# Kernel optimization log

Hardware: AMD Instinct MI355X
Metric: run time of the kernel (lower is better)

## Reference

```python
import jax, jax.numpy as jnp
import numpy as np

IN_FEATURES = 4096
OUT_FEATURES = 11008
GROUP_SIZE = 128
N_HIGH = 1024   # int(0.25*4096)//8*8
N_LOW = 3072    # (4096-1024)//8*8
M_TOKENS = 64


def unpack_6bit(packed, original_k):
    # packed: [K*3//4, N] uint8 values stored as int32
    _, N = packed.shape
    p = packed.reshape(original_k // 4, 3, N)
    b0, b1, b2 = p[:, 0], p[:, 1], p[:, 2]
    v0 = b0 & 63
    v1 = ((b0 >> 6) & 3) | ((b1 & 15) << 2)
    v2 = ((b1 >> 4) & 15) | ((b2 & 3) << 4)
    v3 = (b2 >> 2) & 63
    return jnp.stack([v0, v1, v2, v3], axis=1).reshape(original_k, N)


def unpack_5bit(packed, original_k):
    # packed: [K*5//8, N]
    _, N = packed.shape
    p = packed.reshape(original_k // 8, 5, N)
    b = [p[:, i] for i in range(5)]
    v0 = b[0] & 31
    v1 = ((b[0] >> 5) & 7) | ((b[1] & 3) << 3)
    v2 = (b[1] >> 2) & 31
    v3 = ((b[1] >> 7) & 1) | ((b[2] & 15) << 1)
    v4 = ((b[2] >> 4) & 15) | ((b[3] & 1) << 4)
    v5 = (b[3] >> 1) & 31
    v6 = ((b[3] >> 6) & 3) | ((b[4] & 7) << 2)
    v7 = (b[4] >> 3) & 31
    return jnp.stack([v0, v1, v2, v3, v4, v5, v6, v7], axis=1).reshape(original_k, N)


def dequant_region(W_q, scales, half_range):
    # W_q: [K, N] ints in [0, 2*half_range]; scales: [num_groups, N]
    K, N = W_q.shape
    G = scales.shape[0]
    Wg = (W_q.astype(jnp.float32) - float(half_range)).reshape(G, GROUP_SIZE, N)
    return (Wg * scales[:, None, :]).reshape(K, N)


def setup_inputs() -> dict:
    key = jax.random.key(0)
    ks = jax.random.split(key, 7)
    x = jax.random.normal(ks[0], (M_TOKENS, IN_FEATURES), dtype=jnp.float32)
    W_high_packed = jax.random.randint(ks[1], (N_HIGH * 3 // 4, OUT_FEATURES), 0, 256, dtype=jnp.int32)
    W_low_packed = jax.random.randint(ks[2], (N_LOW * 5 // 8, OUT_FEATURES), 0, 256, dtype=jnp.int32)
    scales_high = jax.random.uniform(ks[3], (N_HIGH // GROUP_SIZE, OUT_FEATURES), dtype=jnp.float32) * 0.02 + 1e-4
    scales_low = jax.random.uniform(ks[4], (N_LOW // GROUP_SIZE, OUT_FEATURES), dtype=jnp.float32) * 0.02 + 1e-4
    col_indices = jax.random.permutation(ks[5], IN_FEATURES).astype(jnp.int32)
    bias = jax.random.normal(ks[6], (OUT_FEATURES,), dtype=jnp.float32) * 0.02
    return {"x": x, "W_high_packed": W_high_packed, "W_low_packed": W_low_packed,
            "scales_high": scales_high, "scales_low": scales_low,
            "col_indices": col_indices, "bias": bias}


def reference(x, W_high_packed, W_low_packed, scales_high, scales_low, col_indices, bias):
    # Unpack mixed 6-bit / 5-bit weights and group-dequantize.
    Wq_high = unpack_6bit(W_high_packed, N_HIGH)          # [1024, N], 0..63
    Wq_low = unpack_5bit(W_low_packed, N_LOW)             # [3072, N], 0..31
    W_high = dequant_region(Wq_high, scales_high, 31)     # 6-bit half_range = 31
    W_low = dequant_region(Wq_low, scales_low, 15)        # 5-bit half_range = 15
    # Column-sensitivity reorder of activations, then split high/low regions.
    x_perm = x[:, col_indices]                            # [M, K]
    x_high = x_perm[:, :N_HIGH]
    x_low = x_perm[:, N_HIGH:N_HIGH + N_LOW]
    out = x_high @ W_high + x_low @ W_low + bias          # [M, N]
    return out
```

## Files before the change

kernel.cpp:

```cpp
#include <hip/hip_runtime.h>


#define NFEAT 11008
#define KTOT  4096

typedef _Float16 half8 __attribute__((ext_vector_type(8)));
typedef float    f32x4 __attribute__((ext_vector_type(4)));

__global__ __launch_bounds__(256) void prep_xfrag(const float* __restrict__ x,
                                                  const int* __restrict__ col,
                                                  _Float16* __restrict__ xfrag) {
    int idx = blockIdx.x * 256 + threadIdx.x;
    int j  = idx & 7;
    int l  = (idx >> 3) & 63;
    int mt = (idx >> 9) & 3;
    int s  = idx >> 11;
    int k  = s * 32 + ((l >> 4) << 3) + j;
    int m  = mt * 16 + (l & 15);
    xfrag[idx] = (_Float16)x[m * KTOT + col[k]];
}

__global__ __launch_bounds__(512) void gemm_kernel(const int* __restrict__ Wh,
                                                   const int* __restrict__ Wl,
                                                   const float* __restrict__ sh,
                                                   const float* __restrict__ sl,
                                                   const _Float16* __restrict__ xfrag,
                                                   float* __restrict__ dst,
                                                   int atomic_mode) {
    const int n0   = blockIdx.x * 64;
    const int kc   = blockIdx.y;
    const int tid  = threadIdx.x;
    const int lane = tid & 63;
    const int wave = tid >> 6;

    __shared__ _Float16 Wfrag[2][8 * 64 * 8 + 4 * 8];

    f32x4 acc[4];
#pragma unroll
    for (int i = 0; i < 4; ++i) acc[i] = (f32x4){0.f, 0.f, 0.f, 0.f};

    const int col  = lane;
    const int nt   = col >> 4;
    const int n_in = col & 15;
    const int kg   = wave;
    const int q_w  = kg >> 2, quad = kg & 3;
    const int woff = (((nt * 2 + q_w) * 64 + quad * 16 + n_in) + nt) * 8;

    const int mt = wave & 3;
    const int qm = wave >> 2;

    auto mfma_step = [&](int t) {
        const int sg = kc * 32 + t * 2 + qm;
        half8 a = *(const half8*)(xfrag + (((sg * 4 + mt) * 64 + lane) << 3));
        const _Float16* wf = Wfrag[t & 1];
#pragma unroll
        for (int j = 0; j < 4; ++j) {
            half8 b = *(const half8*)&wf[(((j * 2 + qm) * 64 + lane) + j) * 8];
            acc[j] = __builtin_amdgcn_mfma_f32_16x16x32_f16(a, b, acc[j], 0, 0, 0);
        }
    };

    if (kc == 0) {
        const int*   base  = Wh + n0 + col;
        const float* sbase = sh + n0 + col;
        int c0, c1, c2, c3, c4, c5; float cs;
        {
            const int* bp = base + 3 * (kg * 2) * NFEAT;
            c0 = bp[0];         c1 = bp[NFEAT];     c2 = bp[2 * NFEAT];
            c3 = bp[3 * NFEAT]; c4 = bp[4 * NFEAT]; c5 = bp[5 * NFEAT];
            cs = sbase[0];
        }
#pragma unroll 2
        for (int t = 0; t < 16; ++t) {
            int n_0 = 0, n_1 = 0, n_2 = 0, n_3 = 0, n_4 = 0, n_5 = 0; float ns = 0.f;
            if (t + 1 < 16) {
                const int G = (t + 1) * 16 + kg * 2;
                const int* bp = base + 3 * G * NFEAT;
                n_0 = bp[0];         n_1 = bp[NFEAT];     n_2 = bp[2 * NFEAT];
                n_3 = bp[3 * NFEAT]; n_4 = bp[4 * NFEAT]; n_5 = bp[5 * NFEAT];
                ns = sbase[((t + 1) >> 1) * NFEAT];
            }
            int v[8];
            v[0] = c0 & 63;
            v[1] = ((c0 >> 6) & 3) | ((c1 & 15) << 2);
            v[2] = ((c1 >> 4) & 15) | ((c2 & 3) << 4);
            v[3] = (c2 >> 2) & 63;
            v[4] = c3 & 63;
            v[5] = ((c3 >> 6) & 3) | ((c4 & 15) << 2);
            v[6] = ((c4 >> 4) & 15) | ((c5 & 3) << 4);
            v[7] = (c5 >> 2) & 63;
            half8 w;
#pragma unroll
            for (int j = 0; j < 8; ++j) w[j] = (_Float16)(((float)v[j] - 31.0f) * cs);
            *(half8*)&Wfrag[t & 1][woff] = w;
            __syncthreads();
            mfma_step(t);
            c0 = n_0; c1 = n_1; c2 = n_2; c3 = n_3; c4 = n_4; c5 = n_5; cs = ns;
        }
    } else {
        const int*   base  = Wl + n0 + col;
        const float* sbase = sl + n0 + col;
        const int Gbase = (kc - 1) * 128;
        const int sbase_row = (kc - 1) * 8;
        int c0, c1, c2, c3, c4; float cs;
        {
            const int* bp = base + 5 * (Gbase + kg) * NFEAT;
            c0 = bp[0]; c1 = bp[NFEAT]; c2 = bp[2 * NFEAT];
            c3 = bp[3 * NFEAT]; c4 = bp[4 * NFEAT];
            cs = sbase[sbase_row * NFEAT];
        }
#pragma unroll 2
        for (int t = 0; t < 16; ++t) {
            int n_0 = 0, n_1 = 0, n_2 = 0, n_3 = 0, n_4 = 0; float ns = 0.f;
            if (t + 1 < 16) {
                const int* bp = base + 5 * (Gbase + (t + 1) * 8 + kg) * NFEAT;
                n_0 = bp[0]; n_1 = bp[NFEAT]; n_2 = bp[2 * NFEAT];
                n_3 = bp[3 * NFEAT]; n_4 = bp[4 * NFEAT];
                ns = sbase[(sbase_row + ((t + 1) >> 1)) * NFEAT];
            }
            int v[8];
            v[0] = c0 & 31;
            v[1] = ((c0 >> 5) & 7) | ((c1 & 3) << 3);
            v[2] = (c1 >> 2) & 31;
            v[3] = ((c1 >> 7) & 1) | ((c2 & 15) << 1);
            v[4] = ((c2 >> 4) & 15) | ((c3 & 1) << 4);
            v[5] = (c3 >> 1) & 31;
            v[6] = ((c3 >> 6) & 3) | ((c4 & 7) << 2);
            v[7] = (c4 >> 3) & 31;
            half8 w;
#pragma unroll
            for (int j = 0; j < 8; ++j) w[j] = (_Float16)(((float)v[j] - 15.0f) * cs);
            *(half8*)&Wfrag[t & 1][woff] = w;
            __syncthreads();
            mfma_step(t);
            c0 = n_0; c1 = n_1; c2 = n_2; c3 = n_3; c4 = n_4; cs = ns;
        }
    }

    __syncthreads();
    float* red = (float*)&Wfrag[0][0];
    if (wave >= 4) {
#pragma unroll
        for (int j = 0; j < 4; ++j)
#pragma unroll
            for (int r = 0; r < 4; ++r)
                red[(j * 4 + r) * 256 + (wave - 4) * 64 + lane] = acc[j][r];
    }
    __syncthreads();
    if (wave < 4) {
#pragma unroll
        for (int j = 0; j < 4; ++j)
#pragma unroll
            for (int r = 0; r < 4; ++r)
                acc[j][r] += red[(j * 4 + r) * 256 + wave * 64 + lane];

        const int rb = wave * 16 + ((lane >> 4) << 2);
        const int cb = lane & 15;
        if (atomic_mode) {
#pragma unroll
            for (int j = 0; j < 4; ++j)
#pragma unroll
                for (int r = 0; r < 4; ++r)
                    atomicAdd(&dst[(rb + r) * NFEAT + n0 + j * 16 + cb], acc[j][r]);
        } else {
            float* base = dst + (size_t)kc * 64 * NFEAT;
#pragma unroll
            for (int j = 0; j < 4; ++j)
#pragma unroll
                for (int r = 0; r < 4; ++r)
                    base[(rb + r) * NFEAT + n0 + j * 16 + cb] = acc[j][r];
        }
    }
}

__global__ __launch_bounds__(256) void reduce_out(const float* __restrict__ part,
                                                  const float* __restrict__ bias,
                                                  float* __restrict__ out) {
    const int idx = blockIdx.x * 256 + threadIdx.x;
    const int f   = idx * 4;
    const int n   = f % NFEAT;
    f32x4 a = *(const f32x4*)(part + f);
    f32x4 b = *(const f32x4*)(part + 704512 + f);
    f32x4 c = *(const f32x4*)(part + 2 * 704512 + f);
    f32x4 d = *(const f32x4*)(part + 3 * 704512 + f);
    f32x4 bi = *(const f32x4*)(bias + n);
    *(f32x4*)(out + f) = a + b + c + d + bi;
}

__global__ __launch_bounds__(256) void init_bias(const float* __restrict__ bias,
                                                 float* __restrict__ out) {
    const int idx = blockIdx.x * 256 + threadIdx.x;
    out[idx] = bias[idx % NFEAT];
}

extern "C" void kernel_launch(void* const* d_in, const int* in_sizes, int n_in,
                              void* d_out, int out_size, void* d_ws, size_t ws_size,
                              hipStream_t stream) {
    const float* x    = (const float*)d_in[0];
    const int*   Wh   = (const int*)d_in[1];
    const int*   Wl   = (const int*)d_in[2];
    const float* sh   = (const float*)d_in[3];
    const float* sl   = (const float*)d_in[4];
    const int*   col  = (const int*)d_in[5];
    const float* bias = (const float*)d_in[6];
    float* out = (float*)d_out;

    _Float16* xfrag = (_Float16*)d_ws;
    const size_t xfrag_bytes = 64 * KTOT * sizeof(_Float16);
    const size_t part_bytes  = 4ull * 64 * NFEAT * sizeof(float);

    prep_xfrag<<<1024, 256, 0, stream>>>(x, col, xfrag);

    dim3 grid(172, 4);
    if (ws_size >= xfrag_bytes + part_bytes) {
        float* part = (float*)((char*)d_ws + xfrag_bytes);
        gemm_kernel<<<grid, 512, 0, stream>>>(Wh, Wl, sh, sl, xfrag, part, 0);
        reduce_out<<<688, 256, 0, stream>>>(part, bias, out);
    } else {
        init_bias<<<2752, 256, 0, stream>>>(bias, out);
        gemm_kernel<<<grid, 512, 0, stream>>>(Wh, Wl, sh, sl, xfrag, out, 1);
    }
}
```

Before: 175.0 us.

## Deepen weight prefetch to two stages and keep global loads in flight across barriers

Restructures the dequant-GEMM main loop into an explicit even/odd two-stage pipeline. Packed weights, scales and x fragments are prefetched two steps ahead instead of one. __syncthreads is replaced by a barrier that waits only on LDS counters, so outstanding global loads stay in flight across the barrier. The aim is to hide global-memory latency for the weight stream, at the cost of more registers and reliance on the LDS double buffer being safe without waiting on vmcnt.

Result: slower. 180.2 us (+3.0%).

```diff
diff --git a/kernel.cpp b/kernel.cpp
--- a/kernel.cpp
+++ b/kernel.cpp
@@ -6,6 +6,13 @@
 
 typedef _Float16 half8 __attribute__((ext_vector_type(8)));
 typedef float    f32x4 __attribute__((ext_vector_type(4)));
+
+#define BARRIER_KEEP_INFLIGHT()                                   \
+    do {                                                          \
+        asm volatile("s_waitcnt lgkmcnt(0)" ::: "memory");        \
+        __builtin_amdgcn_s_barrier();                             \
+        asm volatile("" ::: "memory");                            \
+    } while (0)
 
 __global__ __launch_bounds__(256) void prep_xfrag(const float* __restrict__ x,
                                                   const int* __restrict__ col,
@@ -49,10 +56,10 @@
     const int mt = wave & 3;
     const int qm = wave >> 2;
 
-    auto mfma_step = [&](int t) {
-        const int sg = kc * 32 + t * 2 + qm;
-        half8 a = *(const half8*)(xfrag + (((sg * 4 + mt) * 64 + lane) << 3));
-        const _Float16* wf = Wfrag[t & 1];
+    auto aoff = [&](int t) {
+        return (((kc * 32 + t * 2 + qm) * 4 + mt) * 64 + lane) << 3;
+    };
+    auto mfma4 = [&](const _Float16* wf, half8 a) {
 #pragma unroll
         for (int j = 0; j < 4; ++j) {
             half8 b = *(const half8*)&wf[(((j * 2 + qm) * 64 + lane) + j) * 8];
@@ -61,79 +68,138 @@
     };
 
     if (kc == 0) {
+        auto deq6 = [](int b0, int b1, int b2, int b3, int b4, int b5, float s) -> half8 {
+            int v0 = b0 & 63;
+            int v1 = ((b0 >> 6) & 3) | ((b1 & 15) << 2);
+            int v2 = ((b1 >> 4) & 15) | ((b2 & 3) << 4);
+            int v3 = (b2 >> 2) & 63;
+            int v4 = b3 & 63;
+            int v5 = ((b3 >> 6) & 3) | ((b4 & 15) << 2);
+            int v6 = ((b4 >> 4) & 15) | ((b5 & 3) << 4);
+            int v7 = (b5 >> 2) & 63;
+            half8 w;
+            w[0] = (_Float16)(((float)v0 - 31.0f) * s);
+            w[1] = (_Float16)(((float)v1 - 31.0f) * s);
+            w[2] = (_Float16)(((float)v2 - 31.0f) * s);
+            w[3] = (_Float16)(((float)v3 - 31.0f) * s);
+            w[4] = (_Float16)(((float)v4 - 31.0f) * s);
+            w[5] = (_Float16)(((float)v5 - 31.0f) * s);
+            w[6] = (_Float16)(((float)v6 - 31.0f) * s);
+            w[7] = (_Float16)(((float)v7 - 31.0f) * s);
+            return w;
+        };
         const int*   base  = Wh + n0 + col;
         const float* sbase = sh + n0 + col;
-        int c0, c1, c2, c3, c4, c5; float cs;
+        int A0, A1, A2, A3, A4, A5; float As;
+        int B0, B1, B2, B3, B4, B5; float Bs;
+        half8 xaE, xaO;
         {
             const int* bp = base + 3 * (kg * 2) * NFEAT;
-            c0 = bp[0];         c1 = bp[NFEAT];     c2 = bp[2 * NFEAT];
-            c3 = bp[3 * NFEAT]; c4 = bp[4 * NFEAT]; c5 = bp[5 * NFEAT];
-            cs = sbase[0];
-        }
-#pragma unroll 2
-        for (int t = 0; t < 16; ++t) {
-            int n_0 = 0, n_1 = 0, n_2 = 0, n_3 = 0, n_4 = 0, n_5 = 0; float ns = 0.f;
-            if (t + 1 < 16) {
-                const int G = (t + 1) * 16 + kg * 2;
-                const int* bp = base + 3 * G * NFEAT;
-                n_0 = bp[0];         n_1 = bp[NFEAT];     n_2 = bp[2 * NFEAT];
-                n_3 = bp[3 * NFEAT]; n_4 = bp[4 * NFEAT]; n_5 = bp[5 * NFEAT];
-                ns = sbase[((t + 1) >> 1) * NFEAT];
-            }
-            int v[8];
-            v[0] = c0 & 63;
-            v[1] = ((c0 >> 6) & 3) | ((c1 & 15) << 2);
-            v[2] = ((c1 >> 4) & 15) | ((c2 & 3) << 4);
-            v[3] = (c2 >> 2) & 63;
-            v[4] = c3 & 63;
-            v[5] = ((c3 >> 6) & 3) | ((c4 & 15) << 2);
-            v[6] = ((c4 >> 4) & 15) | ((c5 & 3) << 4);
-            v[7] = (c5 >> 2) & 63;
+            A0 = bp[0];         A1 = bp[NFEAT];     A2 = bp[2 * NFEAT];
+            A3 = bp[3 * NFEAT]; A4 = bp[4 * NFEAT]; A5 = bp[5 * NFEAT];
+            As = sbase[0];
+            bp = base + 3 * (16 + kg * 2) * NFEAT;
+            B0 = bp[0];         B1 = bp[NFEAT];     B2 = bp[2 * NFEAT];
+            B3 = bp[3 * NFEAT]; B4 = bp[4 * NFEAT]; B5 = bp[5 * NFEAT];
+            Bs = sbase[0];
+            xaE = *(const half8*)(xfrag + aoff(0));
+            xaO = *(const half8*)(xfrag + aoff(1));
+        }
+        for (int i = 0; i < 8; ++i) {
+            {
+                half8 w = deq6(A0, A1, A2, A3, A4, A5, As);
+                half8 acur = xaE;
+                *(half8*)&Wfrag[0][woff] = w;
+                const int tp = (i < 7) ? 2 * i + 2 : 14;
+                const int* bp = base + 3 * (tp * 16 + kg * 2) * NFEAT;
+                A0 = bp[0];         A1 = bp[NFEAT];     A2 = bp[2 * NFEAT];
+                A3 = bp[3 * NFEAT]; A4 = bp[4 * NFEAT]; A5 = bp[5 * NFEAT];
+                As = sbase[(tp >> 1) * NFEAT];
+                xaE = *(const half8*)(xfrag + aoff(tp));
+                BARRIER_KEEP_INFLIGHT();
+                mfma4(Wfrag[0], acur);
+            }
+            {
+                half8 w = deq6(B0, B1, B2, B3, B4, B5, Bs);
+                half8 acur = xaO;
+                *(half8*)&Wfrag[1][woff] = w;
+                const int tp = (i < 7) ? 2 * i + 3 : 15;
+                const int* bp = base + 3 * (tp * 16 + kg * 2) * NFEAT;
+                B0 = bp[0];         B1 = bp[NFEAT];     B2 = bp[2 * NFEAT];
+                B3 = bp[3 * NFEAT]; B4 = bp[4 * NFEAT]; B5 = bp[5 * NFEAT];
+                Bs = sbase[(tp >> 1) * NFEAT];
+                xaO = *(const half8*)(xfrag + aoff(tp));
+                BARRIER_KEEP_INFLIGHT();
+                mfma4(Wfrag[1], acur);
+            }
+        }
+    } else {
+        auto deq5 = [](int b0, int b1, int b2, int b3, int b4, float s) -> half8 {
+            int v0 = b0 & 31;
+            int v1 = ((b0 >> 5) & 7) | ((b1 & 3) << 3);
+            int v2 = (b1 >> 2) & 31;
+            int v3 = ((b1 >> 7) & 1) | ((b2 & 15) << 1);
+            int v4 = ((b2 >> 4) & 15) | ((b3 & 1) << 4);
+            int v5 = (b3 >> 1) & 31;
+            int v6 = ((b3 >> 6) & 3) | ((b4 & 7) << 2);
+            int v7 = (b4 >> 3) & 31;
             half8 w;
-#pragma unroll
-            for (int j = 0; j < 8; ++j) w[j] = (_Float16)(((float)v[j] - 31.0f) * cs);
-            *(half8*)&Wfrag[t & 1][woff] = w;
-            __syncthreads();
-            mfma_step(t);
-            c0 = n_0; c1 = n_1; c2 = n_2; c3 = n_3; c4 = n_4; c5 = n_5; cs = ns;
-        }
-    } else {
+            w[0] = (_Float16)(((float)v0 - 15.0f) * s);
+            w[1] = (_Float16)(((float)v1 - 15.0f) * s);
+            w[2] = (_Float16)(((float)v2 - 15.0f) * s);
+            w[3] = (_Float16)(((float)v3 - 15.0f) * s);
+            w[4] = (_Float16)(((float)v4 - 15.0f) * s);
+            w[5] = (_Float16)(((float)v5 - 15.0f) * s);
+            w[6] = (_Float16)(((float)v6 - 15.0f) * s);
+            w[7] = (_Float16)(((float)v7 - 15.0f) * s);
+            return w;
+        };
         const int*   base  = Wl + n0 + col;
         const float* sbase = sl + n0 + col;
-        const int Gbase = (kc - 1) * 128;
+        const int Gbase     = (kc - 1) * 128;
         const int sbase_row = (kc - 1) * 8;
-        int c0, c1, c2, c3, c4; float cs;
+        int A0, A1, A2, A3, A4; float As;
+        int B0, B1, B2, B3, B4; float Bs;
+        half8 xaE, xaO;
         {
             const int* bp = base + 5 * (Gbase + kg) * NFEAT;
-            c0 = bp[0]; c1 = bp[NFEAT]; c2 = bp[2 * NFEAT];
-            c3 = bp[3 * NFEAT]; c4 = bp[4 * NFEAT];
-            cs = sbase[sbase_row * NFEAT];
-        }
-#pragma unroll 2
-        for (int t = 0; t < 16; ++t) {
-            int n_0 = 0, n_1 = 0, n_2 = 0, n_3 = 0, n_4 = 0; float ns = 0.f;
-            if (t + 1 < 16) {
-                const int* bp = base + 5 * (Gbase + (t + 1) * 8 + kg) * NFEAT;
-                n_0 = bp[0]; n_1 = bp[NFEAT]; n_2 = bp[2 * NFEAT];
-                n_3 = bp[3 * NFEAT]; n_4 = bp[4 * NFEAT];
-                ns = sbase[(sbase_row + ((t + 1) >> 1)) * NFEAT];
-            }
-            int v[8];
-            v[0] = c0 & 31;
-            v[1] = ((c0 >> 5) & 7) | ((c1 & 3) << 3);
-            v[2] = (c1 >> 2) & 31;
-            v[3] = ((c1 >> 7) & 1) | ((c2 & 15) << 1);
-            v[4] = ((c2 >> 4) & 15) | ((c3 & 1) << 4);
-            v[5] = (c3 >> 1) & 31;
-            v[6] = ((c3 >> 6) & 3) | ((c4 & 7) << 2);
-            v[7] = (c4 >> 3) & 31;
-            half8 w;
-#pragma unroll
-            for (int j = 0; j < 8; ++j) w[j] = (_Float16)(((float)v[j] - 15.0f) * cs);
-            *(half8*)&Wfrag[t & 1][woff] = w;
-            __syncthreads();
-            mfma_step(t);
-            c0 = n_0; c1 = n_1; c2 = n_2; c3 = n_3; c4 = n_4; cs = ns;
+            A0 = bp[0]; A1 = bp[NFEAT]; A2 = bp[2 * NFEAT];
+            A3 = bp[3 * NFEAT]; A4 = bp[4 * NFEAT];
+            As = sbase[sbase_row * NFEAT];
+            bp = base + 5 * (Gbase + 8 + kg) * NFEAT;
+            B0 = bp[0]; B1 = bp[NFEAT]; B2 = bp[2 * NFEAT];
+            B3 = bp[3 * NFEAT]; B4 = bp[4 * NFEAT];
+            Bs = sbase[sbase_row * NFEAT];
+            xaE = *(const half8*)(xfrag + aoff(0));
+            xaO = *(const half8*)(xfrag + aoff(1));
+        }
+        for (int i = 0; i < 8; ++i) {
+            {
+                half8 w = deq5(A0, A1, A2, A3, A4, As);
+                half8 acur = xaE;
+                *(half8*)&Wfrag[0][woff] = w;
+                const int tp = (i < 7) ? 2 * i + 2 : 14;
+                const int* bp = base + 5 * (Gbase + tp * 8 + kg) * NFEAT;
+                A0 = bp[0]; A1 = bp[NFEAT]; A2 = bp[2 * NFEAT];
+                A3 = bp[3 * NFEAT]; A4 = bp[4 * NFEAT];
+                As = sbase[(sbase_row + (tp >> 1)) * NFEAT];
+                xaE = *(const half8*)(xfrag + aoff(tp));
+                BARRIER_KEEP_INFLIGHT();
+                mfma4(Wfrag[0], acur);
+            }
+            {
+                half8 w = deq5(B0, B1, B2, B3, B4, Bs);
+                half8 acur = xaO;
+                *(half8*)&Wfrag[1][woff] = w;
+                const int tp = (i < 7) ? 2 * i + 3 : 15;
+                const int* bp = base + 5 * (Gbase + tp * 8 + kg) * NFEAT;
+                B0 = bp[0]; B1 = bp[NFEAT]; B2 = bp[2 * NFEAT];
+                B3 = bp[3 * NFEAT]; B4 = bp[4 * NFEAT];
+                Bs = sbase[(sbase_row + (tp >> 1)) * NFEAT];
+                xaO = *(const half8*)(xfrag + aoff(tp));
+                BARRIER_KEEP_INFLIGHT();
+                mfma4(Wfrag[1], acur);
+            }
         }
     }
 
```
